# Optimization experiments

Measured on AMD Instinct MI355X. Metric: run time of the kernel, lower is better.

## Reference

```python
import jax, jax.numpy as jnp
import numpy as np

N_R = 256          # number of relations
N_HOP_MAX = 3      # max hops
N_E = 200_000      # number of entities
N_T = 1_000_000    # number of KB triples
B = 32             # batch size
D_Q = 768          # BERT question embedding dim
D_IN = D_Q + (N_HOP_MAX - 1) * N_R  # input width of dense_inf / dense_att


def setup_inputs() -> dict:
    key = jax.random.key(0)
    ks = jax.random.split(key, 7)
    x = (jax.random.uniform(ks[0], (B, N_E)) < 0.001).astype(jnp.float32)
    h_q = jax.random.normal(ks[1], (B, D_Q), jnp.float32)
    W_inf = jax.random.normal(ks[2], (N_R, D_IN), jnp.float32) * 0.02
    W_att = jax.random.normal(ks[3], (1, D_IN), jnp.float32) * 0.02
    subj_idx = jax.random.randint(ks[4], (N_T,), 0, N_E, jnp.int32)
    rel_idx = jax.random.randint(ks[5], (N_T,), 0, N_R, jnp.int32)
    obj_idx = jax.random.randint(ks[6], (N_T,), 0, N_E, jnp.int32)
    return {"x": x, "h_q": h_q, "W_inf": W_inf, "W_att": W_att,
            "subj_idx": subj_idx, "rel_idx": rel_idx, "obj_idx": obj_idx,
            "n_hop": N_HOP_MAX}


def _one_step(x, r, subj_idx, rel_idx, obj_idx):
    # Equivalent to ((x @ M_subj.T) * (r @ M_rel.T)) @ M_obj with 0/1
    # indicator matrices: gather - elementwise multiply - scatter-add.
    x_t = jnp.take(x, subj_idx, axis=1)   # (B, N_T)
    r_t = jnp.take(r, rel_idx, axis=1)    # (B, N_T)
    prod = x_t * r_t                       # (B, N_T)
    # scatter-add over triples into object entities: (N_T, B) -> (N_E, B)
    return jax.ops.segment_sum(prod.T, obj_idx, num_segments=x.shape[1]).T


def reference(x, h_q, W_inf, W_att, subj_idx, rel_idx, obj_idx, n_hop):
    rs, cs, xs = [], [], []
    for i in range(n_hop):
        if i:
            # most-recent relation first, then older ones (rs[::-1])
            concat = jnp.concatenate([h_q] + rs[::-1], axis=1)
        else:
            concat = h_q
        pad = jnp.zeros((h_q.shape[0], (N_HOP_MAX - 1 - i) * N_R), h_q.dtype)
        concat = jnp.concatenate([concat, pad], axis=1)  # (B, D_IN)
        r = concat @ W_inf.T   # (B, N_R)
        c = concat @ W_att.T   # (B, 1)
        x = _one_step(x, r, subj_idx, rel_idx, obj_idx)  # (B, N_E)
        rs.append(r)
        cs.append(c)
        xs.append(x)
    a = jax.nn.softmax(jnp.concatenate(cs, axis=1), axis=-1)  # (B, n_hop)
    y = jnp.einsum('bh,bhe->be', a, jnp.stack(xs, axis=1))     # (B, N_E)
    return y
```

## Files before the change

kernel.cpp:

```cpp
#include <hip/hip_runtime.h>

#define N_R   256
#define N_E   200000
#define N_T   1000000
#define B     32
#define D_Q   768
#define D_IN  1280

__global__ void k_mask0(const float* __restrict__ x, unsigned* __restrict__ mask0) {
    int e = blockIdx.x * 256 + threadIdx.x;
    if (e >= N_E) return;
    unsigned m = 0;
#pragma unroll 8
    for (int b = 0; b < 32; ++b)
        m |= (x[(size_t)b * N_E + e] != 0.f ? 1u : 0u) << b;
    mask0[e] = m;
}

__global__ void k_r0(const float* __restrict__ h_q, const float* __restrict__ W_inf,
                     float* __restrict__ rT0) {
    __shared__ float hs[32 * 257];
    __shared__ float red[256];
    int t = threadIdx.x, rel = blockIdx.x;
    int b = t & 31, kp = t >> 5;
    float acc = 0.f;
    for (int c = 0; c < 3; ++c) {
        __syncthreads();
#pragma unroll
        for (int i = 0; i < 32; ++i)
            hs[i * 257 + t] = h_q[i * D_Q + c * 256 + t];
        __syncthreads();
        const float* w = &W_inf[rel * D_IN + c * 256 + kp * 32];
#pragma unroll
        for (int i = 0; i < 32; ++i)
            acc += w[i] * hs[b * 257 + kp * 32 + i];
    }
    red[t] = acc;
    __syncthreads();
    if (t < 32) {
        float s = 0.f;
        for (int q = 0; q < 8; ++q) s += red[q * 32 + t];
        rT0[rel * 32 + t] = s;
    }
}

__global__ void k_r12(const float* __restrict__ W_inf, const float* __restrict__ rT0,
                      const float* __restrict__ rPrev, float* __restrict__ rOut,
                      int hop2) {
    __shared__ float red[256];
    int t = threadIdx.x, rel = blockIdx.x;
    int b = t & 31, jp = t >> 5;
    const float* w2 = &W_inf[rel * D_IN + D_Q];
    float acc = 0.f;
#pragma unroll 8
    for (int jj = 0; jj < 32; ++jj) {
        int j = jp * 32 + jj;
        acc += w2[j] * rPrev[j * 32 + b];
    }
    if (hop2) {
        const float* w3 = w2 + N_R;
#pragma unroll 8
        for (int jj = 0; jj < 32; ++jj) {
            int j = jp * 32 + jj;
            acc += w3[j] * rT0[j * 32 + b];
        }
    }
    red[t] = acc;
    __syncthreads();
    if (t < 32) {
        float s = rT0[rel * 32 + t];
        for (int q = 0; q < 8; ++q) s += red[q * 32 + t];
        rOut[rel * 32 + t] = s;
    }
}

__global__ void k_att(const float* __restrict__ h_q, const float* __restrict__ W_att,
                      const float* __restrict__ rT0, const float* __restrict__ rT1,
                      float* __restrict__ a_w) {
    __shared__ float p0[256], p1[256], p2[256], p3[256];
    int t = threadIdx.x;
    int b = t & 31, p = t >> 5;
    float c0 = 0.f;
    for (int k = p * 96; k < p * 96 + 96; ++k) c0 += W_att[k] * h_q[b * D_Q + k];
    float s1 = 0.f, s2 = 0.f, s3 = 0.f;
    for (int j = p * 32; j < p * 32 + 32; ++j) {
        float w2 = W_att[D_Q + j], w3 = W_att[D_Q + N_R + j];
        float r0v = rT0[j * 32 + b], r1v = rT1[j * 32 + b];
        s1 += w2 * r0v; s2 += w2 * r1v; s3 += w3 * r0v;
    }
    p0[t] = c0; p1[t] = s1; p2[t] = s2; p3[t] = s3;
    __syncthreads();
    if (t < 32) {
        float C0 = 0.f, S1 = 0.f, S2 = 0.f, S3 = 0.f;
        for (int q = 0; q < 8; ++q) {
            C0 += p0[q * 32 + t]; S1 += p1[q * 32 + t];
            S2 += p2[q * 32 + t]; S3 += p3[q * 32 + t];
        }
        float c1 = C0 + S1, c2 = C0 + S2 + S3;
        float m  = fmaxf(C0, fmaxf(c1, c2));
        float e0 = __expf(C0 - m), e1 = __expf(c1 - m), e2 = __expf(c2 - m);
        float inv = 1.f / (e0 + e1 + e2);
        a_w[t] = e0 * inv; a_w[32 + t] = e1 * inv; a_w[64 + t] = e2 * inv;
    }
}

template <bool BN_LAYOUT, bool HAS_NEXT>
__global__ void k_hop(const float* __restrict__ xIn,
                      const unsigned* __restrict__ maskIn,
                      const float* __restrict__ rT, const float* __restrict__ aw,
                      const int* __restrict__ subj, const int* __restrict__ rel,
                      const int* __restrict__ obj,
                      float* __restrict__ xOut, unsigned* __restrict__ maskOut,
                      float* __restrict__ outp) {
    int i = blockIdx.x * 256 + threadIdx.x;
    if (i >= N_T) return;
    int s = subj[i];
    unsigned m = maskIn[s];
    if (!m) return;
    int r = rel[i];
    int o = obj[i];
    const float* rrow = rT + r * 32;
    unsigned mm = m;
    while (mm) {
        int b = __ffs(mm) - 1;
        mm &= mm - 1;
        float v = BN_LAYOUT ? xIn[(size_t)b * N_E + s] : xIn[s * 32 + b];
        float c = v * rrow[b];
        if (HAS_NEXT) unsafeAtomicAdd(&xOut[o * 32 + b], c);
        unsafeAtomicAdd(&outp[(size_t)b * N_E + o], aw[b] * c);
    }
    if (HAS_NEXT) atomicOr(&maskOut[o], m);
}

extern "C" void kernel_launch(void* const* d_in, const int* in_sizes, int n_in,
                              void* d_out, int out_size, void* d_ws, size_t ws_size,
                              hipStream_t stream) {
    const float* x     = (const float*)d_in[0];
    const float* h_q   = (const float*)d_in[1];
    const float* W_inf = (const float*)d_in[2];
    const float* W_att = (const float*)d_in[3];
    const int*   subj  = (const int*)d_in[4];
    const int*   rel   = (const int*)d_in[5];
    const int*   obj   = (const int*)d_in[6];
    float* out = (float*)d_out;

    const size_t NEB = (size_t)N_E * B;
    float*    bufA  = (float*)d_ws;
    float*    bufB  = bufA + NEB;
    float*    rT    = bufB + NEB;
    float*    a_w   = rT + 3 * N_R * B;
    unsigned* mask1 = (unsigned*)(a_w + 96);
    unsigned* mask2 = mask1 + N_E;
    unsigned* mask0 = mask2 + N_E;

    const int EB  = (N_E + 255) / 256;
    const int TBL = (N_T + 255) / 256;

    hipMemsetAsync(bufA, 0, 2 * NEB * sizeof(float), stream);
    hipMemsetAsync(mask1, 0, 2 * N_E * sizeof(unsigned), stream);
    hipMemsetAsync(out, 0, NEB * sizeof(float), stream);

    k_mask0<<<EB, 256, 0, stream>>>(x, mask0);

    k_r0 <<<N_R, 256, 0, stream>>>(h_q, W_inf, rT);
    k_r12<<<N_R, 256, 0, stream>>>(W_inf, rT, rT, rT + N_R * B, 0);
    k_r12<<<N_R, 256, 0, stream>>>(W_inf, rT, rT + N_R * B, rT + 2 * N_R * B, 1);
    k_att<<<1, 256, 0, stream>>>(h_q, W_att, rT, rT + N_R * B, a_w);

    k_hop<true, true><<<TBL, 256, 0, stream>>>(x, mask0, rT, a_w,
                                               subj, rel, obj, bufA, mask1, out);
    k_hop<false, true><<<TBL, 256, 0, stream>>>(bufA, mask1, rT + N_R * B, a_w + 32,
                                                subj, rel, obj, bufB, mask2, out);
    k_hop<false, false><<<TBL, 256, 0, stream>>>(bufB, mask2, rT + 2 * N_R * B, a_w + 64,
                                                 subj, rel, obj, (float*)0,
                                                 (unsigned*)0, out);
}
```

Before: 215.9 us.

## Fuse zeroing into mask prep, merge relation chain, vectorize triple loads

```diff
diff --git a/kernel.cpp b/kernel.cpp
--- a/kernel.cpp
+++ b/kernel.cpp
@@ -7,14 +7,27 @@
 #define D_Q   768
 #define D_IN  1280
 
-__global__ void k_mask0(const float* __restrict__ x, unsigned* __restrict__ mask0) {
-    int e = blockIdx.x * 256 + threadIdx.x;
-    if (e >= N_E) return;
-    unsigned m = 0;
+__global__ void k_prep(const float* __restrict__ x, unsigned* __restrict__ mask0,
+                       unsigned* __restrict__ mask1, unsigned* __restrict__ mask2,
+                       float4* __restrict__ bufs ,
+                       float4* __restrict__ outv) {
+    int tid = blockIdx.x * 256 + threadIdx.x;
+    float4 z = {0.f, 0.f, 0.f, 0.f};
+#pragma unroll
+    for (int i = 0; i < 4; ++i)
+        bufs[(size_t)i * 800000 + tid] = z;
+#pragma unroll
+    for (int i = 0; i < 2; ++i)
+        outv[(size_t)i * 800000 + tid] = z;
+    if (tid < N_E) {
+        unsigned m = 0;
 #pragma unroll 8
-    for (int b = 0; b < 32; ++b)
-        m |= (x[(size_t)b * N_E + e] != 0.f ? 1u : 0u) << b;
-    mask0[e] = m;
+        for (int b = 0; b < 32; ++b)
+            m |= (x[(size_t)b * N_E + tid] != 0.f ? 1u : 0u) << b;
+        mask0[tid] = m;
+        mask1[tid] = 0u;
+        mask2[tid] = 0u;
+    }
 }
 
 __global__ void k_r0(const float* __restrict__ h_q, const float* __restrict__ W_inf,
@@ -44,63 +57,79 @@
     }
 }
 
-__global__ void k_r12(const float* __restrict__ W_inf, const float* __restrict__ rT0,
-                      const float* __restrict__ rPrev, float* __restrict__ rOut,
-                      int hop2) {
-    __shared__ float red[256];
-    int t = threadIdx.x, rel = blockIdx.x;
-    int b = t & 31, jp = t >> 5;
-    const float* w2 = &W_inf[rel * D_IN + D_Q];
-    float acc = 0.f;
-#pragma unroll 8
-    for (int jj = 0; jj < 32; ++jj) {
-        int j = jp * 32 + jj;
-        acc += w2[j] * rPrev[j * 32 + b];
-    }
-    if (hop2) {
-        const float* w3 = w2 + N_R;
-#pragma unroll 8
-        for (int jj = 0; jj < 32; ++jj) {
-            int j = jp * 32 + jj;
-            acc += w3[j] * rT0[j * 32 + b];
-        }
-    }
-    red[t] = acc;
+__global__ void __launch_bounds__(1024) k_rchain(
+        const float* __restrict__ W_inf, const float* __restrict__ W_att,
+        const float* __restrict__ h_q, const float* __restrict__ rT0g,
+        float* __restrict__ rT1g, float* __restrict__ rT2g,
+        float* __restrict__ a_wg) {
+    __shared__ float r0s[8192];
+    __shared__ float r1s[8192];
+    __shared__ float red[1024];
+    __shared__ float a0s[32], a1s[32], a2s[32];
+    int t = threadIdx.x;
+    int b = t & 31, g = t >> 5;
+
+    for (int i = t; i < 8192; i += 1024) r0s[i] = rT0g[i];
+    __syncthreads();
+
+    float r1v[8];
+#pragma unroll
+    for (int k = 0; k < 8; ++k) {
+        int rel = g * 8 + k;
+        const float* w2 = W_inf + rel * D_IN + D_Q;
+        float acc = r0s[rel * 32 + b];
+        for (int j = 0; j < N_R; ++j) acc += w2[j] * r0s[j * 32 + b];
+        r1v[k] = acc;
+    }
+#pragma unroll
+    for (int k = 0; k < 8; ++k) {
+        r1s[(g * 8 + k) * 32 + b] = r1v[k];
+        rT1g[(g * 8 + k) * 32 + b] = r1v[k];
+    }
+    __syncthreads();
+
+    float p0 = 0.f;
+    for (int k = g * 24; k < g * 24 + 24; ++k) p0 += W_att[k] * h_q[b * D_Q + k];
+    float p1 = 0.f, p2 = 0.f, p3 = 0.f;
+    for (int j = g * 8; j < g * 8 + 8; ++j) {
+        float w2 = W_att[D_Q + j], w3 = W_att[D_Q + N_R + j];
+        p1 += w2 * r0s[j * 32 + b];
+        p2 += w2 * r1s[j * 32 + b];
+        p3 += w3 * r0s[j * 32 + b];
+    }
+    float C0 = 0.f, S1 = 0.f, S2 = 0.f, S3 = 0.f;
+    red[t] = p0; __syncthreads();
+    if (t < 32) for (int q = 0; q < 32; ++q) C0 += red[q * 32 + t];
+    __syncthreads();
+    red[t] = p1; __syncthreads();
+    if (t < 32) for (int q = 0; q < 32; ++q) S1 += red[q * 32 + t];
+    __syncthreads();
+    red[t] = p2; __syncthreads();
+    if (t < 32) for (int q = 0; q < 32; ++q) S2 += red[q * 32 + t];
+    __syncthreads();
+    red[t] = p3; __syncthreads();
+    if (t < 32) for (int q = 0; q < 32; ++q) S3 += red[q * 32 + t];
     __syncthreads();
     if (t < 32) {
-        float s = rT0[rel * 32 + t];
-        for (int q = 0; q < 8; ++q) s += red[q * 32 + t];
-        rOut[rel * 32 + t] = s;
-    }
-}
-
-__global__ void k_att(const float* __restrict__ h_q, const float* __restrict__ W_att,
-                      const float* __restrict__ rT0, const float* __restrict__ rT1,
-                      float* __restrict__ a_w) {
-    __shared__ float p0[256], p1[256], p2[256], p3[256];
-    int t = threadIdx.x;
-    int b = t & 31, p = t >> 5;
-    float c0 = 0.f;
-    for (int k = p * 96; k < p * 96 + 96; ++k) c0 += W_att[k] * h_q[b * D_Q + k];
-    float s1 = 0.f, s2 = 0.f, s3 = 0.f;
-    for (int j = p * 32; j < p * 32 + 32; ++j) {
-        float w2 = W_att[D_Q + j], w3 = W_att[D_Q + N_R + j];
-        float r0v = rT0[j * 32 + b], r1v = rT1[j * 32 + b];
-        s1 += w2 * r0v; s2 += w2 * r1v; s3 += w3 * r0v;
-    }
-    p0[t] = c0; p1[t] = s1; p2[t] = s2; p3[t] = s3;
-    __syncthreads();
-    if (t < 32) {
-        float C0 = 0.f, S1 = 0.f, S2 = 0.f, S3 = 0.f;
-        for (int q = 0; q < 8; ++q) {
-            C0 += p0[q * 32 + t]; S1 += p1[q * 32 + t];
-            S2 += p2[q * 32 + t]; S3 += p3[q * 32 + t];
-        }
         float c1 = C0 + S1, c2 = C0 + S2 + S3;
         float m  = fmaxf(C0, fmaxf(c1, c2));
         float e0 = __expf(C0 - m), e1 = __expf(c1 - m), e2 = __expf(c2 - m);
         float inv = 1.f / (e0 + e1 + e2);
-        a_w[t] = e0 * inv; a_w[32 + t] = e1 * inv; a_w[64 + t] = e2 * inv;
+        a0s[t] = e0 * inv; a1s[t] = e1 * inv; a2s[t] = e2 * inv;
+        a_wg[t] = e0 * inv; a_wg[32 + t] = e1 * inv; a_wg[64 + t] = e2 * inv;
+    }
+    __syncthreads();
+
+    float a2 = a2s[b];
+#pragma unroll
+    for (int k = 0; k < 8; ++k) {
+        int rel = g * 8 + k;
+        const float* w2 = W_inf + rel * D_IN + D_Q;
+        const float* w3 = w2 + N_R;
+        float acc = r0s[rel * 32 + b];
+        for (int j = 0; j < N_R; ++j)
+            acc += w2[j] * r1s[j * 32 + b] + w3[j] * r0s[j * 32 + b];
+        rT2g[rel * 32 + b] = a2 * acc;
     }
 }
 
@@ -108,28 +137,42 @@
 __global__ void k_hop(const float* __restrict__ xIn,
                       const unsigned* __restrict__ maskIn,
                       const float* __restrict__ rT, const float* __restrict__ aw,
-                      const int* __restrict__ subj, const int* __restrict__ rel,
-                      const int* __restrict__ obj,
+                      const int4* __restrict__ subj4, const int4* __restrict__ rel4,
+                      const int4* __restrict__ obj4,
                       float* __restrict__ xOut, unsigned* __restrict__ maskOut,
                       float* __restrict__ outp) {
-    int i = blockIdx.x * 256 + threadIdx.x;
-    if (i >= N_T) return;
-    int s = subj[i];
-    unsigned m = maskIn[s];
-    if (!m) return;
-    int r = rel[i];
-    int o = obj[i];
-    const float* rrow = rT + r * 32;
-    unsigned mm = m;
-    while (mm) {
-        int b = __ffs(mm) - 1;
-        mm &= mm - 1;
-        float v = BN_LAYOUT ? xIn[(size_t)b * N_E + s] : xIn[s * 32 + b];
-        float c = v * rrow[b];
-        if (HAS_NEXT) unsafeAtomicAdd(&xOut[o * 32 + b], c);
-        unsafeAtomicAdd(&outp[(size_t)b * N_E + o], aw[b] * c);
-    }
-    if (HAS_NEXT) atomicOr(&maskOut[o], m);
+    int tid = blockIdx.x * 256 + threadIdx.x;
+    if (tid >= N_T / 4) return;
+    int4 s4 = subj4[tid];
+    unsigned m0 = maskIn[s4.x], m1 = maskIn[s4.y];
+    unsigned m2 = maskIn[s4.z], m3 = maskIn[s4.w];
+    if (!(m0 | m1 | m2 | m3)) return;
+    int4 r4 = rel4[tid];
+    int4 o4 = obj4[tid];
+    int      ss[4] = {s4.x, s4.y, s4.z, s4.w};
+    unsigned mk[4] = {m0, m1, m2, m3};
+    int      rr[4] = {r4.x, r4.y, r4.z, r4.w};
+    int      oo[4] = {o4.x, o4.y, o4.z, o4.w};
+#pragma unroll
+    for (int k = 0; k < 4; ++k) {
+        unsigned mm = mk[k];
+        if (!mm) continue;
+        int s = ss[k], o = oo[k];
+        const float* rrow = rT + rr[k] * 32;
+        while (mm) {
+            int b = __ffs(mm) - 1;
+            mm &= mm - 1;
+            float v = BN_LAYOUT ? xIn[(size_t)b * N_E + s] : xIn[s * 32 + b];
+            float c = v * rrow[b];
+            if (HAS_NEXT) {
+                unsafeAtomicAdd(&xOut[o * 32 + b], c);
+                unsafeAtomicAdd(&outp[(size_t)b * N_E + o], aw[b] * c);
+            } else {
+                unsafeAtomicAdd(&outp[(size_t)b * N_E + o], c);
+            }
+        }
+        if (HAS_NEXT) atomicOr(&maskOut[o], mk[k]);
+    }
 }
 
 extern "C" void kernel_launch(void* const* d_in, const int* in_sizes, int n_in,
@@ -149,29 +192,29 @@
     float*    bufB  = bufA + NEB;
     float*    rT    = bufB + NEB;
     float*    a_w   = rT + 3 * N_R * B;
-    unsigned* mask1 = (unsigned*)(a_w + 96);
+    unsigned* mask0 = (unsigned*)(a_w + 96);
+    unsigned* mask1 = mask0 + N_E;
     unsigned* mask2 = mask1 + N_E;
-    unsigned* mask0 = mask2 + N_E;
-
-    const int EB  = (N_E + 255) / 256;
-    const int TBL = (N_T + 255) / 256;
-
-    hipMemsetAsync(bufA, 0, 2 * NEB * sizeof(float), stream);
-    hipMemsetAsync(mask1, 0, 2 * N_E * sizeof(unsigned), stream);
-    hipMemsetAsync(out, 0, NEB * sizeof(float), stream);
-
-    k_mask0<<<EB, 256, 0, stream>>>(x, mask0);
-
-    k_r0 <<<N_R, 256, 0, stream>>>(h_q, W_inf, rT);
-    k_r12<<<N_R, 256, 0, stream>>>(W_inf, rT, rT, rT + N_R * B, 0);
-    k_r12<<<N_R, 256, 0, stream>>>(W_inf, rT, rT + N_R * B, rT + 2 * N_R * B, 1);
-    k_att<<<1, 256, 0, stream>>>(h_q, W_att, rT, rT + N_R * B, a_w);
-
-    k_hop<true, true><<<TBL, 256, 0, stream>>>(x, mask0, rT, a_w,
-                                               subj, rel, obj, bufA, mask1, out);
-    k_hop<false, true><<<TBL, 256, 0, stream>>>(bufA, mask1, rT + N_R * B, a_w + 32,
-                                                subj, rel, obj, bufB, mask2, out);
-    k_hop<false, false><<<TBL, 256, 0, stream>>>(bufB, mask2, rT + 2 * N_R * B, a_w + 64,
-                                                 subj, rel, obj, (float*)0,
-                                                 (unsigned*)0, out);
-}
+
+    const int PB  = 3125;
+    const int HB  = (N_T / 4 + 255) / 256;
+
+    k_prep<<<PB, 256, 0, stream>>>(x, mask0, mask1, mask2,
+                                   (float4*)bufA, (float4*)out);
+
+    k_r0    <<<N_R, 256, 0, stream>>>(h_q, W_inf, rT);
+    k_rchain<<<1, 1024, 0, stream>>>(W_inf, W_att, h_q, rT,
+                                     rT + N_R * B, rT + 2 * N_R * B, a_w);
+
+    k_hop<true, true><<<HB, 256, 0, stream>>>(x, mask0, rT, a_w,
+                                              (const int4*)subj, (const int4*)rel,
+                                              (const int4*)obj, bufA, mask1, out);
+    k_hop<false, true><<<HB, 256, 0, stream>>>(bufA, mask1, rT + N_R * B, a_w + 32,
+                                               (const int4*)subj, (const int4*)rel,
+                                               (const int4*)obj, bufB, mask2, out);
+    k_hop<false, false><<<HB, 256, 0, stream>>>(bufB, mask2, rT + 2 * N_R * B,
+                                                (const float*)0,
+                                                (const int4*)subj, (const int4*)rel,
+                                                (const int4*)obj, (float*)0,
+                                                (unsigned*)0, out);
+}
```

New measurement: 402.3 us. 86.3% more time.
